# Optimization experiments

Hardware: AMD Instinct MI355X
Metric: run time of the kernel (lower is better)

The kernel has to match this reference:

```python
import jax, jax.numpy as jnp
import numpy as np

PS, R, FS, SS = 3, 2, 3, 10.0
PAD = (PS - 1) // 2  # 1


def extract_patches(x, ps, stride):
    # x: (C, Hp, Wp) already padded -> (C, ps, ps, ho, wo)
    C, Hp, Wp = x.shape
    ho = (Hp - ps) // stride + 1
    wo = (Wp - ps) // stride + 1
    rows = []
    for i in range(ps):
        cols = []
        for j in range(ps):
            cols.append(x[:, i:i + stride * ho:stride, j:j + stride * wo:stride])
        rows.append(jnp.stack(cols, axis=1))
    return jnp.stack(rows, axis=1)


def fuse_diag(S):
    # conv2d of (L,L) 'image' with eye(3) kernel, zero pad 1:
    # out[u,v] = S[u-1,v-1] + S[u,v] + S[u+1,v+1]
    Sp = jnp.pad(S, 1)
    return Sp[:-2, :-2] + Sp[1:-1, 1:-1] + Sp[2:, 2:]


def ca_single(f, b, mask):
    # f, b: (c, h, w); mask: (1, h, w)
    c, h, w = f.shape
    # full-res background patches (replicate pad, stride R) -> reconstruction bank
    b_pad = jnp.pad(b, ((0, 0), (PAD, PAD), (PAD, PAD)), mode='edge')
    bg = extract_patches(b_pad, PS, R)                 # (c,ps,ps,hr,wr)
    hr, wr = bg.shape[3], bg.shape[4]
    L = hr * wr
    bg = bg.reshape(c, PS, PS, L).transpose(3, 0, 1, 2)  # (L,c,ps,ps)
    # nearest 1/R downsample (F.interpolate nearest == strided pick)
    fl = f[:, ::R, ::R]
    bl = b[:, ::R, ::R]
    ml = mask[:, ::R, ::R]
    # shrunk background patches (replicate pad, stride 1) -> matching bank
    bl_pad = jnp.pad(bl, ((0, 0), (PAD, PAD), (PAD, PAD)), mode='edge')
    bgs = extract_patches(bl_pad, PS, 1).reshape(c, PS, PS, L).transpose(3, 0, 1, 2)
    # mask patches (zero pad), valid iff patch mean == 0
    mp = extract_patches(jnp.pad(ml, ((0, 0), (PAD, PAD), (PAD, PAD))), PS, 1)
    mi = (mp.mean(axis=(1, 2)).reshape(L) == 0.0).astype(f.dtype)  # (L,)
    # L2-normalize matching patches (clamped at 1e-4)
    bnorm = jnp.maximum(jnp.sqrt((bgs ** 2).sum(axis=(1, 2, 3))), 1e-4)
    bgs_n = bgs / bnorm[:, None, None, None]
    # score = conv2d(f, patches) with zero pad 1 -> cosine-like correlation
    fp = extract_patches(jnp.pad(fl, ((0, 0), (PAD, PAD), (PAD, PAD))), PS, 1)
    score = jnp.einsum('cijhw,lcij->lhw', fp, bgs_n)   # (L,hr,wr)
    # two-pass diagonal 'fuse' trick
    S = fuse_diag(score.reshape(L, L))
    S = S.reshape(hr, wr, hr, wr).transpose(1, 0, 3, 2).reshape(L, L)
    S = fuse_diag(S)
    score = S.reshape(wr, hr, wr, hr).transpose(1, 0, 3, 2).reshape(L, hr, wr)
    # masked softmax over the L patch axis
    score = score * mi[:, None, None]
    score = jax.nn.softmax(score * SS, axis=0) * mi[:, None, None]
    # conv_transpose2d(score, bg, stride=R, padding=PAD) / 4
    # == conv of R-dilated score with flipped kernel, pad = PS-1-PAD
    w_flip = bg[:, :, ::-1, ::-1].transpose(1, 0, 2, 3)  # (c,L,ps,ps)
    out = jax.lax.conv_general_dilated(
        score[None], w_flip, window_strides=(1, 1),
        padding=[(PS - 1 - PAD, PS - 1 - PAD)] * 2, lhs_dilation=(R, R),
        dimension_numbers=('NCHW', 'OIHW', 'NCHW'))[0] / 4.0  # (c,2hr-1,2wr-1)
    if out.shape[1] % 2 == 1:  # static shape check, matches torch branch
        out = jnp.pad(out, ((0, 0), (0, 1), (0, 1)), mode='edge')
    return out


def setup_inputs() -> dict:
    key = jax.random.key(0)
    k1, k2, k3 = jax.random.split(key, 3)
    B, c, h, w = 4, 128, 128, 128
    f = jax.random.normal(k1, (B, c, h, w), dtype=jnp.float32)
    b = jax.random.normal(k2, (B, c, h, w), dtype=jnp.float32)
    mask = jax.random.bernoulli(k3, 0.25, (B, 1, h, w)).astype(jnp.float32)
    return {'f': f, 'b': b, 'mask': mask}


def reference(f, b, mask):
    return jax.vmap(ca_single)(f, b, mask)
```

## Files before the change

### kernel.cpp

```cpp
#include <hip/hip_runtime.h>
#include <cstdint>

#define LVAL 4096
#define K1 1152
#define NT1 18
#define CCH 128
#define HH 128
#define WW 128
#define SSCALE 10.0f
#define NUPAD 2048
#define NACTPAD 512
#define PADPIX 4356
#define PIMG 557568

typedef __attribute__((ext_vector_type(8))) short short8;
typedef __attribute__((ext_vector_type(8))) _Float16 half8;
typedef __attribute__((ext_vector_type(4))) float f32x4;

static __device__ __forceinline__ int clampi(int v, int lo, int hi) {
    return v < lo ? lo : (v > hi ? hi : v);
}
static __device__ __forceinline__ unsigned short f2h(float x) {
    union { _Float16 h; unsigned short u; } c; c.h = (_Float16)x; return c.u;
}
static __device__ __forceinline__ float h2f(unsigned short u) {
    union { _Float16 h; unsigned short u; } c; c.u = u; return (float)c.h;
}

__global__ __launch_bounds__(256) void dst_kernel(const float* __restrict__ f,
        const float* __restrict__ b, unsigned short* __restrict__ fpad4,
        unsigned short* __restrict__ bpad4) {
    __shared__ float t[32][65];
    int h = blockIdx.x;
    int cg = blockIdx.y;
    int za = blockIdx.z;
    int img = za >> 1, arr = za & 1;
    const float* src = (arr ? b : f) + (size_t)img * CCH * HH * WW;
    unsigned short* dst = (arr ? bpad4 : fpad4) + (size_t)img * PIMG;
    int tid = threadIdx.x;
    int w = tid & 63, csub = tid >> 6;
    #pragma unroll
    for (int cc = 0; cc < 8; ++cc) {
        int cl = csub * 8 + cc;
        int ch = cg * 32 + cl;
        t[cl][w] = src[(size_t)ch * (HH * WW) + (2 * h) * WW + (2 * w)];
    }
    __syncthreads();
    int c = tid & 31, pr = tid >> 5;
    #pragma unroll
    for (int pp = 0; pp < 8; ++pp) {
        int w2 = pr * 8 + pp;
        dst[((size_t)(h + 1) * 66 + (w2 + 1)) * 128 + cg * 32 + c] = f2h(t[c][w2]);
    }
}

__global__ __launch_bounds__(256) void qk_border_kernel(unsigned short* __restrict__ fpad4,
        unsigned short* __restrict__ bpad4, float* __restrict__ Q) {
    int img = blockIdx.y;
    int tid = threadIdx.x;
    if (blockIdx.x < 1024) {
        int lane = tid & 63, sub = tid >> 6;
        int pix = blockIdx.x * 4 + sub;
        const unsigned short* row = bpad4 + (size_t)img * PIMG
                                    + ((size_t)((pix >> 6) + 1) * 66 + (pix & 63) + 1) * 128;
        uint32_t hv = *(const uint32_t*)(row + lane * 2);
        float a = h2f((unsigned short)(hv & 0xffff));
        float b2 = h2f((unsigned short)(hv >> 16));
        float s = a * a + b2 * b2;
        for (int off = 32; off > 0; off >>= 1) s += __shfl_xor(s, off, 64);
        if (lane == 0) Q[img * 4096 + pix] = s;
    } else {
        int id = (blockIdx.x - 1024) * 256 + tid;
        if (id >= PADPIX * 16) return;
        int pix = id >> 4, cg = (id & 15) << 3;
        int hp = pix / 66, wp = pix - hp * 66;
        if (hp >= 1 && hp <= 64 && wp >= 1 && wp <= 64) return;
        unsigned short* fp = fpad4 + (size_t)img * PIMG + (size_t)pix * 128 + cg;
        #pragma unroll
        for (int cc = 0; cc < 8; ++cc) fp[cc] = 0;
        int hs = clampi(hp - 1, 0, 63), wsx = clampi(wp - 1, 0, 63);
        const unsigned short* sb = bpad4 + (size_t)img * PIMG
                                   + ((size_t)(hs + 1) * 66 + (wsx + 1)) * 128 + cg;
        unsigned short* bp = bpad4 + (size_t)img * PIMG + (size_t)pix * 128 + cg;
        #pragma unroll
        for (int cc = 0; cc < 8; ++cc) bp[cc] = sb[cc];
    }
}

__global__ __launch_bounds__(1024) void compact_kernel(const float* __restrict__ mask,
        const float* __restrict__ Q, int* __restrict__ act, int* __restrict__ ulist,
        short* __restrict__ tapu, float* __restrict__ invn, int* __restrict__ hdr) {
    int img = blockIdx.x;
    const float* mk = mask + (size_t)img * HH * WW;
    const float* Qi = Q + img * 4096;
    int* acti = act + img * NACTPAD;
    int* uli = ulist + img * NUPAD;
    short* tpi = tapu + (size_t)img * NACTPAD * 12;
    float* invi = invn + (size_t)img * NUPAD;
    int* hd = hdr + img * 4;
    int tid = threadIdx.x;
    int lane = tid & 63, wv = tid >> 6;
    __shared__ unsigned char flag[4096];
    __shared__ short umap[4096];
    __shared__ int actl[NACTPAD];
    __shared__ float ssl[4096];
    __shared__ int wsum[16], woff[16];
    __shared__ int tot;

    int loc[4];
    int cnt = 0;
    #pragma unroll
    for (int k = 0; k < 4; ++k) {
        int a = tid * 4 + k;
        int hb = a >> 6, wb = a & 63;
        float s = 0.f;
        for (int di = -1; di <= 1; ++di)
            for (int dj = -1; dj <= 1; ++dj) {
                int hh = hb + di, w2 = wb + dj;
                if (hh >= 0 && hh < 64 && w2 >= 0 && w2 < 64)
                    s += mk[(2 * hh) * WW + 2 * w2];
            }
        loc[k] = (s == 0.f) ? 1 : 0;
        cnt += loc[k];
    }
    int pre = cnt;
    for (int off = 1; off < 64; off <<= 1) { int v = __shfl_up(pre, off, 64); if (lane >= off) pre += v; }
    if (lane == 63) wsum[wv] = pre;
    __syncthreads();
    if (tid == 0) { int a2 = 0; for (int w2 = 0; w2 < 16; ++w2) { woff[w2] = a2; a2 += wsum[w2]; } tot = a2; }
    __syncthreads();
    int base = woff[wv] + pre - cnt;
    int n_act = tot < NACTPAD ? tot : NACTPAD;
    {
        int p = base;
        #pragma unroll
        for (int k = 0; k < 4; ++k)
            if (loc[k]) { if (p < NACTPAD) { acti[p] = tid * 4 + k; actl[p] = tid * 4 + k; } p++; }
    }
    #pragma unroll
    for (int k = 0; k < 4; ++k) { flag[tid * 4 + k] = 0; umap[tid * 4 + k] = -1; }
    __syncthreads();
    for (int j = tid; j < n_act; j += 1024) {
        int a = actl[j];
        int sa = ((a & 63) << 6) + (a >> 6);
        #pragma unroll
        for (int ei = 0; ei < 3; ++ei) {
            int tbt = sa + ei - 1;
            if (tbt < 0 || tbt >= 4096) continue;
            int tb = ((tbt & 63) << 6) + (tbt >> 6);
            #pragma unroll
            for (int d = -1; d <= 1; ++d) {
                int rb = tb + d;
                if (rb >= 0 && rb < 4096) flag[rb] = 1;
            }
        }
    }
    __syncthreads();
    int cnt2 = 0;
    int loc2[4];
    #pragma unroll
    for (int k = 0; k < 4; ++k) { loc2[k] = flag[tid * 4 + k]; cnt2 += loc2[k]; }
    int pre2 = cnt2;
    for (int off = 1; off < 64; off <<= 1) { int v = __shfl_up(pre2, off, 64); if (lane >= off) pre2 += v; }
    if (lane == 63) wsum[wv] = pre2;
    __syncthreads();
    if (tid == 0) { int a2 = 0; for (int w2 = 0; w2 < 16; ++w2) { woff[w2] = a2; a2 += wsum[w2]; } tot = a2; }
    __syncthreads();
    int base2 = woff[wv] + pre2 - cnt2;
    int n_u = tot < NUPAD ? tot : NUPAD;
    {
        int p = base2;
        #pragma unroll
        for (int k = 0; k < 4; ++k)
            if (loc2[k]) { int ci = tid * 4 + k; if (p < NUPAD) { uli[p] = ci; umap[ci] = (short)p; } p++; }
    }
    __syncthreads();
    for (int j = tid; j < n_act; j += 1024) {
        int a = actl[j];
        int sa = ((a & 63) << 6) + (a >> 6);
        #pragma unroll
        for (int ei = 0; ei < 3; ++ei) {
            int tbt = sa + ei - 1;
            int ok = (tbt >= 0 && tbt < 4096);
            int tb = ok ? ((tbt & 63) << 6) + (tbt >> 6) : 0;
            #pragma unroll
            for (int d = -1; d <= 1; ++d) {
                short v = -1;
                if (ok) { int rb = tb + d; if (rb >= 0 && rb < 4096) v = umap[rb]; }
                tpi[j * 12 + ei * 3 + d + 1] = v;
            }
        }
    }
    for (int a = tid; a < 4096; a += 1024) {
        int hb = a >> 6, wb = a & 63;
        float s = 0.f;
        #pragma unroll
        for (int i = 0; i < 3; ++i)
            #pragma unroll
            for (int j2 = 0; j2 < 3; ++j2) {
                int hl = clampi(hb + i - 1, 0, 63);
                int wl = clampi(wb + j2 - 1, 0, 63);
                s += Qi[hl * 64 + wl];
            }
        ssl[a] = s;
    }
    for (int u = tid; u < NUPAD; u += 1024) invi[u] = 0.f;
    __syncthreads();
    for (int ci = tid; ci < 4096; ci += 1024) {
        if (flag[ci]) {
            int u = umap[ci];
            if (u >= 0) invi[u] = 1.f / fmaxf(sqrtf(ssl[ci]), 1e-4f);
        }
    }
    if (tid == 0) { hd[0] = n_act; hd[1] = n_u; }
}

__global__ void prep_bgtc_kernel(const float* __restrict__ b, const int* __restrict__ act,
                                 const int* __restrict__ hdr, unsigned short* __restrict__ BGTc4) {
    int gimg = blockIdx.y;
    const float* bi = b + (size_t)gimg * CCH * HH * WW;
    int idx = blockIdx.x * 256 + threadIdx.x;
    int k2 = idx >> 9, j = idx & 511;
    int n_act = hdr[gimg * 4];
    unsigned short v = 0;
    if (j < n_act) {
        int a = act[gimg * NACTPAD + j];
        int ch = k2 & 127, q = k2 >> 7;
        int i = q / 3, jj = q - i * 3;
        int y = clampi(2 * (a >> 6) + i - 1, 0, 127);
        int x = clampi(2 * (a & 63) + jj - 1, 0, 127);
        v = f2h(bi[(size_t)ch * (HH * WW) + y * WW + x]);
    }
    BGTc4[(size_t)gimg * K1 * NACTPAD + idx] = v;
}

#define BAR() __builtin_amdgcn_s_barrier()
#define WAITV6() asm volatile("s_waitcnt vmcnt(6)" ::: "memory")
#define WAITV0() asm volatile("s_waitcnt vmcnt(0)" ::: "memory")

#define STAGEX(tt, h) do {                                                              \
    int t_ = (tt);                                                                      \
    if (t_ < NT1) {                                                                     \
        const int isB_ = ((h) == 1 || (h) == 2);                                        \
        const int hi_ = ((h) >= 2) ? 1 : 0;                                             \
        int q_ = t_ >> 1;                                                               \
        int qi_ = (q_ * 11) >> 5;                                                       \
        int qj_ = q_ - qi_ * 3;                                                         \
        int toff_ = ((qi_ * 66 + qj_) << 7) + ((t_ & 1) << 6);                          \
        _Pragma("unroll")                                                               \
        for (int r_ = 0; r_ < 2; ++r_) {                                                \
            int sl_ = hi_ * 2 + r_;                                                     \
            const unsigned short* g_ = (isB_ ? bR[sl_] : aR[sl_]) + toff_;              \
            unsigned short* l_ = lds + (isB_ ? 32768 : 0) + ((t_ & 1) << 14)            \
                                 + ((hi_ * 128 + r_ * 64 + swb) << 6);                  \
            __builtin_amdgcn_global_load_lds((const uint32_t*)(const void*)g_,          \
                                             (uint32_t*)(void*)l_, 16, 0, 0);           \
        }                                                                               \
    } } while (0)

#define LDA4(cur, ah) do {                                                              \
    _Pragma("unroll")                                                                   \
    for (int f_ = 0; f_ < 4; ++f_)                                                      \
    { _Pragma("unroll")                                                                 \
      for (int s_ = 0; s_ < 2; ++s_) {                                                  \
        int row_ = wm * 128 + ((ah) * 4 + f_) * 16 + row16;                             \
        int cs_ = ((s_ << 2) + kgrp) ^ (row16 & 7);                                     \
        av[f_ * 2 + s_] = *(const half8*)(lds + ((cur) << 14) + (row_ << 6) + (cs_ << 3)); \
    } } } while (0)

#define LDB2(cur, bh) do {                                                              \
    _Pragma("unroll")                                                                   \
    for (int f_ = 0; f_ < 2; ++f_)                                                      \
    { _Pragma("unroll")                                                                 \
      for (int s_ = 0; s_ < 2; ++s_) {                                                  \
        int row_ = wn * 64 + ((bh) * 2 + f_) * 16 + row16;                              \
        int cs_ = ((s_ << 2) + kgrp) ^ (row16 & 7);                                     \
        bv[(bh) * 4 + f_ * 2 + s_] = *(const half8*)(lds + 32768 + ((cur) << 14) + (row_ << 6) + (cs_ << 3)); \
    } } } while (0)

#define MFMA16(ai, bj) do {                                                             \
    __builtin_amdgcn_s_setprio(1);                                                      \
    _Pragma("unroll")                                                                   \
    for (int f_ = 0; f_ < 4; ++f_)                                                      \
    { _Pragma("unroll")                                                                 \
      for (int g_ = 0; g_ < 2; ++g_)                                                    \
      { _Pragma("unroll")                                                               \
        for (int s_ = 0; s_ < 2; ++s_)                                                  \
            acc[(ai) * 4 + f_][(bj) * 2 + g_] = __builtin_amdgcn_mfma_f32_16x16x32_f16( \
                av[f_ * 2 + s_], bv[(bj) * 4 + g_ * 2 + s_], acc[(ai) * 4 + f_][(bj) * 2 + g_], 0, 0, 0); \
    } } __builtin_amdgcn_s_setprio(0); } while (0)

__global__ __launch_bounds__(512, 2) void gemm1_8phase(const unsigned short* __restrict__ fpad4,
        const unsigned short* __restrict__ bpad4, unsigned short* __restrict__ Scc4,
        const int* __restrict__ ulist, const int* __restrict__ hdr,
        const float* __restrict__ invn) {
    __shared__ unsigned short lds[65536];
    const int gimg = blockIdx.y;
    const unsigned short* fpadI = fpad4 + (size_t)gimg * PIMG;
    const unsigned short* bpadI = bpad4 + (size_t)gimg * PIMG;
    unsigned short* C = Scc4 + (size_t)gimg * 4096 * NUPAD;
    const int* uli = ulist + gimg * NUPAD;
    const float* invi = invn + (size_t)gimg * NUPAD;
    const int n_u = hdr[gimg * 4 + 1];
    const int tid = threadIdx.x;
    const int lane = tid & 63;
    const int wave = tid >> 6;
    const int wm = wave >> 2, wn = wave & 3;
    const int row16 = lane & 15, kgrp = lane >> 4;
    const int srow = tid >> 3, schunk = tid & 7;
    const int swb = wave << 3;
    int bid = blockIdx.x;
    int wgid = ((bid & 7) << 4) + (bid >> 3);
    const int bm = (wgid >> 3) << 8;
    const int bn = (wgid & 7) << 8;
    if (bn >= ((n_u + 255) & ~255)) return;

    const int ck8 = (schunk ^ (srow & 7)) << 3;
    const unsigned short* aR[4];
    const unsigned short* bR[4];
    #pragma unroll
    for (int i2 = 0; i2 < 4; ++i2) {
        int rowp = i2 * 64 + srow;
        int ar = bm + rowp;
        aR[i2] = fpadI + (size_t)((ar >> 6) * 66 + (ar & 63)) * 128 + ck8;
        int uu = bn + rowp;
        int brow = uli[uu < n_u ? uu : n_u - 1];
        bR[i2] = bpadI + (size_t)((brow >> 6) * 66 + (brow & 63)) * 128 + ck8;
    }

    f32x4 acc[8][4];
    #pragma unroll
    for (int i = 0; i < 8; ++i)
        #pragma unroll
        for (int j = 0; j < 4; ++j)
            acc[i][j] = (f32x4){0.f, 0.f, 0.f, 0.f};

    STAGEX(0, 1); STAGEX(0, 2); STAGEX(0, 0); STAGEX(0, 3);
    STAGEX(1, 1); STAGEX(1, 2); STAGEX(1, 0);
    WAITV6();
    BAR();

    half8 av[8], bv[8];
    for (int t = 0; t < NT1; ++t) {
        const int cur = t & 1;
        LDA4(cur, 0);
        LDB2(cur, 0);
        LDB2(cur, 1);
        STAGEX(t + 1, 3);
        BAR();
        MFMA16(0, 0);
        BAR();
        STAGEX(t + 2, 1);
        BAR();
        MFMA16(0, 1);
        BAR();
        LDA4(cur, 1);
        STAGEX(t + 2, 2);
        BAR();
        MFMA16(1, 0);
        BAR();
        STAGEX(t + 2, 0);
        BAR();
        MFMA16(1, 1);
        if (t >= NT1 - 2) { WAITV0(); } else { WAITV6(); }
        BAR();
    }

    float iv[4];
    #pragma unroll
    for (int fj = 0; fj < 4; ++fj)
        iv[fj] = invi[bn + wn * 64 + fj * 16 + row16];
    #pragma unroll
    for (int fi = 0; fi < 8; ++fi) {
        int crow = bm + wm * 128 + fi * 16 + kgrp * 4;
        #pragma unroll
        for (int fj = 0; fj < 4; ++fj) {
            int ccol = bn + wn * 64 + fj * 16 + row16;
            f32x4 v = acc[fi][fj];
            #pragma unroll
            for (int r = 0; r < 4; ++r)
                C[(size_t)(crow + r) * NUPAD + ccol] = f2h(v[r] * iv[fj]);
        }
    }
}

__global__ __launch_bounds__(512) void fuse_softmax_kernel(const unsigned short* __restrict__ Scc4,
        const int* __restrict__ hdr, const short* __restrict__ tapu,
        unsigned short* __restrict__ Pc4) {
    __shared__ unsigned short lrow[3][NUPAD];
    __shared__ float redm[8], reds[8];
    int gimg = blockIdx.y;
    const unsigned short* Scc = Scc4 + (size_t)gimg * 4096 * NUPAD;
    int bid = blockIdx.x;
    int sb = ((bid & 7) << 9) + (bid >> 3);
    int b = ((sb & 63) << 6) + (sb >> 6);
    int tid = threadIdx.x;
    int lane = tid & 63, wv = tid >> 6;
    int n_act = hdr[gimg * 4];
    int n_u = hdr[gimg * 4 + 1];
    int nu_s = (n_u + 15) & ~15;
    if (nu_s > NUPAD) nu_s = NUPAD;
    int rvalid = 0;
    int ra_[9];
    #pragma unroll
    for (int ei = 0; ei < 3; ++ei) {
        int tt = sb + ei - 1;
        int ok = (tt >= 0 && tt < 4096);
        int ta = ok ? ((tt & 63) << 6) + (tt >> 6) : 0;
        #pragma unroll
        for (int dp = 0; dp < 3; ++dp) {
            int ra = ta + dp - 1;
            int t = ei * 3 + dp;
            ra_[t] = ra;
            if (ok && ra >= 0 && ra < 4096) rvalid |= 1 << t;
        }
    }
    bool actv = tid < n_act;
    short tp[9];
    if (actv) {
        const short* tpp = tapu + ((size_t)gimg * NACTPAD + tid) * 12;
        #pragma unroll
        for (int t = 0; t < 9; ++t) tp[t] = tpp[t];
    }
    float s = 0.f;
    #pragma unroll
    for (int ei = 0; ei < 3; ++ei) {
        #pragma unroll
        for (int dp = 0; dp < 3; ++dp) {
            int t = ei * 3 + dp;
            if ((rvalid >> t) & 1) {
                const unsigned short* src = Scc + (size_t)ra_[t] * NUPAD;
                for (int u = tid * 8; u < nu_s; u += 4096)
                    *(uint4*)&lrow[dp][u] = *(const uint4*)(src + u);
            }
        }
        __syncthreads();
        if (actv) {
            #pragma unroll
            for (int dp = 0; dp < 3; ++dp) {
                int t = ei * 3 + dp;
                if ((rvalid >> t) & 1) {
                    int u = tp[t];
                    if (u >= 0) s += h2f(lrow[dp][u]);
                }
            }
        }
        __syncthreads();
    }
    float l = actv ? SSCALE * s : 0.f;
    float x = actv ? l : -3.0e38f;
    for (int off = 32; off > 0; off >>= 1) x = fmaxf(x, __shfl_xor(x, off, 64));
    if (lane == 0) redm[wv] = x;
    __syncthreads();
    float m = -3.0e38f;
    #pragma unroll
    for (int w2 = 0; w2 < 8; ++w2) m = fmaxf(m, redm[w2]);
    m = fmaxf(m, 0.f);
    float e = actv ? __expf(l - m) : 0.f;
    float sm = e;
    for (int off = 32; off > 0; off >>= 1) sm += __shfl_xor(sm, off, 64);
    if (lane == 0) reds[wv] = sm;
    __syncthreads();
    float S = 0.f;
    #pragma unroll
    for (int w2 = 0; w2 < 8; ++w2) S += reds[w2];
    float denom = S + (4096.f - (float)n_act) * __expf(-m);
    Pc4[(size_t)gimg * 4096 * NACTPAD + (size_t)b * NACTPAD + tid] = f2h(actv ? e / denom : 0.f);
}

__global__ __launch_bounds__(256) void gemm2_nt(
        const unsigned short* __restrict__ BGTc4, const unsigned short* __restrict__ Pc4,
        const int* __restrict__ hdr, unsigned short* __restrict__ OUTT4) {
    __shared__ unsigned short lds[2 * 128 * 64];
    unsigned short* Asm = lds;
    unsigned short* Bsm = lds + 128 * 64;
    const int gimg = blockIdx.z;
    const unsigned short* A = BGTc4 + (size_t)gimg * K1 * NACTPAD;
    const unsigned short* B = Pc4 + (size_t)gimg * 4096 * NACTPAD;
    unsigned short* C = OUTT4 + (size_t)gimg * K1 * LVAL;
    int n_act = hdr[gimg * 4];
    int kend = (n_act + 63) & ~63;
    if (kend < 64) kend = 64;
    const int tid = threadIdx.x;
    const int wave = tid >> 6, lane = tid & 63;
    const int wm = wave >> 1, wn = wave & 1;
    const int bm = blockIdx.y << 7, bn = blockIdx.x << 7;
    const int rsub = lane >> 3, csub = lane & 7;
    const int gcol = (csub ^ rsub) << 3;
    const int row16 = lane & 15, kgrp = lane >> 4;
    const int sw = (row16 & 7) << 3;

    f32x4 acc[4][4];
    #pragma unroll
    for (int i = 0; i < 4; ++i)
        #pragma unroll
        for (int j = 0; j < 4; ++j)
            acc[i][j] = (f32x4){0.f, 0.f, 0.f, 0.f};

    for (int k0 = 0; k0 < kend; k0 += 64) {
        __syncthreads();
        #pragma unroll
        for (int r = 0; r < 4; ++r) {
            int row = (wave << 5) + (r << 3) + rsub;
            const unsigned short* ga = A + (size_t)(bm + row) * NACTPAD + k0 + gcol;
            unsigned short* la = Asm + (((wave << 5) + (r << 3)) << 6);
            __builtin_amdgcn_global_load_lds((const uint32_t*)(const void*)ga,
                                             (uint32_t*)(void*)la, 16, 0, 0);
            const unsigned short* gb = B + (size_t)(bn + row) * NACTPAD + k0 + gcol;
            unsigned short* lb = Bsm + (((wave << 5) + (r << 3)) << 6);
            __builtin_amdgcn_global_load_lds((const uint32_t*)(const void*)gb,
                                             (uint32_t*)(void*)lb, 16, 0, 0);
        }
        __syncthreads();
        #pragma unroll
        for (int s = 0; s < 2; ++s) {
            half8 af[4], bfr[4];
            #pragma unroll
            for (int fi = 0; fi < 4; ++fi) {
                int ar = (wm << 6) + (fi << 4) + row16;
                af[fi] = *(const half8*)(Asm + (ar << 6) + (((s << 5) + (kgrp << 3)) ^ sw));
            }
            #pragma unroll
            for (int fj = 0; fj < 4; ++fj) {
                int br = (wn << 6) + (fj << 4) + row16;
                bfr[fj] = *(const half8*)(Bsm + (br << 6) + (((s << 5) + (kgrp << 3)) ^ sw));
            }
            #pragma unroll
            for (int fi = 0; fi < 4; ++fi)
                #pragma unroll
                for (int fj = 0; fj < 4; ++fj)
                    acc[fi][fj] = __builtin_amdgcn_mfma_f32_16x16x32_f16(
                        af[fi], bfr[fj], acc[fi][fj], 0, 0, 0);
        }
        __syncthreads();
    }
    #pragma unroll
    for (int fi = 0; fi < 4; ++fi) {
        int crow = bm + (wm << 6) + (fi << 4) + (kgrp << 2);
        #pragma unroll
        for (int fj = 0; fj < 4; ++fj) {
            int ccol = bn + (wn << 6) + (fj << 4) + row16;
            f32x4 v = acc[fi][fj];
            #pragma unroll
            for (int r = 0; r < 4; ++r)
                C[(size_t)(crow + r) * LVAL + ccol] = f2h(v[r]);
        }
    }
}

__global__ void scatter_kernel(const unsigned short* __restrict__ OUTT4,
                               float* __restrict__ out) {
    int gimg = blockIdx.y;
    const unsigned short* OUTT = OUTT4 + (size_t)gimg * K1 * LVAL;
    float* oi = out + (size_t)gimg * CCH * HH * WW;
    int idx = blockIdx.x * 256 + threadIdx.x;
    int x = idx & 127;
    int y = (idx >> 7) & 127;
    int ch = idx >> 14;
    int yy = y < 127 ? y : 126;
    int xx = x < 127 ? x : 126;
    int hy[2], iy[2], ny;
    if (yy & 1) { hy[0] = (yy + 1) >> 1; iy[0] = 0; hy[1] = (yy - 1) >> 1; iy[1] = 2; ny = 2; }
    else        { hy[0] = yy >> 1;       iy[0] = 1; ny = 1; }
    int wx[2], jx[2], nx;
    if (xx & 1) { wx[0] = (xx + 1) >> 1; jx[0] = 0; wx[1] = (xx - 1) >> 1; jx[1] = 2; nx = 2; }
    else        { wx[0] = xx >> 1;       jx[0] = 1; nx = 1; }
    float s = 0.f;
    for (int u = 0; u < ny; ++u)
        for (int v = 0; v < nx; ++v) {
            int k2 = (iy[u] * 3 + jx[v]) * 128 + ch;
            s += h2f(OUTT[(size_t)k2 * LVAL + (hy[u] << 6) + wx[v]]);
        }
    oi[idx] = s * 0.25f;
}

extern "C" void kernel_launch(void* const* d_in, const int* in_sizes, int n_in,
                              void* d_out, int out_size, void* d_ws, size_t ws_size,
                              hipStream_t stream) {
    const float* f = (const float*)d_in[0];
    const float* b = (const float*)d_in[1];
    const float* mask = (const float*)d_in[2];
    float* out = (float*)d_out;
    char* ws = (char*)d_ws;

    const size_t oQ    = 0;
    const size_t oACT  = 65536;
    const size_t oUL   = 73728;
    const size_t oTAP  = 106496;
    const size_t oHDR  = 155648;
    const size_t oINVN = 156672;
    const size_t oBGTC = 189440;
    const size_t oPC   = 4908032;
    const size_t oFPAD = 21685248;
    const size_t oBPAD = 26145792;
    const size_t oSCC  = 30606336;

    float* Q   = (float*)(ws + oQ);
    int*   ACT = (int*)(ws + oACT);
    int*   UL  = (int*)(ws + oUL);
    short* TAP = (short*)(ws + oTAP);
    int*   HDR = (int*)(ws + oHDR);
    float* INVN = (float*)(ws + oINVN);
    unsigned short* BGTc4 = (unsigned short*)(ws + oBGTC);
    unsigned short* Pc4   = (unsigned short*)(ws + oPC);
    unsigned short* fpad4 = (unsigned short*)(ws + oFPAD);
    unsigned short* bpad4 = (unsigned short*)(ws + oBPAD);
    unsigned short* Scc4 = (unsigned short*)(ws + oSCC);
    unsigned short* OUTT4 = (unsigned short*)(ws + oSCC);

    dst_kernel<<<dim3(64, 4, 8), 256, 0, stream>>>(f, b, fpad4, bpad4);
    qk_border_kernel<<<dim3(1297, 4), 256, 0, stream>>>(fpad4, bpad4, Q);
    compact_kernel<<<4, 1024, 0, stream>>>(mask, Q, ACT, UL, TAP, INVN, HDR);
    prep_bgtc_kernel<<<dim3(2304, 4), 256, 0, stream>>>(b, ACT, HDR, BGTc4);

    gemm1_8phase<<<dim3(128, 4), 512, 0, stream>>>(fpad4, bpad4, Scc4, UL, HDR, INVN);
    fuse_softmax_kernel<<<dim3(4096, 4), 512, 0, stream>>>(Scc4, HDR, TAP, Pc4);

    gemm2_nt<<<dim3(32, 9, 4), 256, 0, stream>>>(BGTc4, Pc4, HDR, OUTT4);
    scatter_kernel<<<dim3(8192, 4), 256, 0, stream>>>(OUTT4, out);
    (void)in_sizes; (void)n_in; (void)out_size; (void)ws_size;
}
```

Baseline: 242.8 us.

## Process four output rows per fuse-softmax block and double-buffer A fragments in gemm1

Measured after the change: 222.7 us. -8.3%, faster.

```diff
diff --git a/kernel.cpp b/kernel.cpp
--- a/kernel.cpp
+++ b/kernel.cpp
@@ -258,14 +258,14 @@
         }                                                                               \
     } } while (0)
 
-#define LDA4(cur, ah) do {                                                              \
+#define LDA4(dst, cur, ah) do {                                                         \
     _Pragma("unroll")                                                                   \
     for (int f_ = 0; f_ < 4; ++f_)                                                      \
     { _Pragma("unroll")                                                                 \
       for (int s_ = 0; s_ < 2; ++s_) {                                                  \
         int row_ = wm * 128 + ((ah) * 4 + f_) * 16 + row16;                             \
         int cs_ = ((s_ << 2) + kgrp) ^ (row16 & 7);                                     \
-        av[f_ * 2 + s_] = *(const half8*)(lds + ((cur) << 14) + (row_ << 6) + (cs_ << 3)); \
+        dst[f_ * 2 + s_] = *(const half8*)(lds + ((cur) << 14) + (row_ << 6) + (cs_ << 3)); \
     } } } while (0)
 
 #define LDB2(cur, bh) do {                                                              \
@@ -278,7 +278,7 @@
         bv[(bh) * 4 + f_ * 2 + s_] = *(const half8*)(lds + 32768 + ((cur) << 14) + (row_ << 6) + (cs_ << 3)); \
     } } } while (0)
 
-#define MFMA16(ai, bj) do {                                                             \
+#define MFMA16(va, ai, bj) do {                                                         \
     __builtin_amdgcn_s_setprio(1);                                                      \
     _Pragma("unroll")                                                                   \
     for (int f_ = 0; f_ < 4; ++f_)                                                      \
@@ -287,7 +287,7 @@
       { _Pragma("unroll")                                                               \
         for (int s_ = 0; s_ < 2; ++s_)                                                  \
             acc[(ai) * 4 + f_][(bj) * 2 + g_] = __builtin_amdgcn_mfma_f32_16x16x32_f16( \
-                av[f_ * 2 + s_], bv[(bj) * 4 + g_ * 2 + s_], acc[(ai) * 4 + f_][(bj) * 2 + g_], 0, 0, 0); \
+                va[f_ * 2 + s_], bv[(bj) * 4 + g_ * 2 + s_], acc[(ai) * 4 + f_][(bj) * 2 + g_], 0, 0, 0); \
     } } __builtin_amdgcn_s_setprio(0); } while (0)
 
 __global__ __launch_bounds__(512, 2) void gemm1_8phase(const unsigned short* __restrict__ fpad4,
@@ -340,28 +340,28 @@
     WAITV6();
     BAR();
 
-    half8 av[8], bv[8];
+    half8 av0[8], av1[8], bv[8];
     for (int t = 0; t < NT1; ++t) {
         const int cur = t & 1;
-        LDA4(cur, 0);
+        LDA4(av0, cur, 0);
         LDB2(cur, 0);
         LDB2(cur, 1);
         STAGEX(t + 1, 3);
         BAR();
-        MFMA16(0, 0);
+        MFMA16(av0, 0, 0);
+        LDA4(av1, cur, 1);
         BAR();
         STAGEX(t + 2, 1);
         BAR();
-        MFMA16(0, 1);
-        BAR();
-        LDA4(cur, 1);
+        MFMA16(av0, 0, 1);
+        BAR();
         STAGEX(t + 2, 2);
         BAR();
-        MFMA16(1, 0);
+        MFMA16(av1, 1, 0);
         BAR();
         STAGEX(t + 2, 0);
         BAR();
-        MFMA16(1, 1);
+        MFMA16(av1, 1, 1);
         if (t >= NT1 - 2) { WAITV0(); } else { WAITV6(); }
         BAR();
     }
@@ -388,33 +388,17 @@
         const int* __restrict__ hdr, const short* __restrict__ tapu,
         unsigned short* __restrict__ Pc4) {
     __shared__ unsigned short lrow[3][NUPAD];
-    __shared__ float redm[8], reds[8];
+    __shared__ float redm[8][4], reds[8][4];
     int gimg = blockIdx.y;
     const unsigned short* Scc = Scc4 + (size_t)gimg * 4096 * NUPAD;
     int bid = blockIdx.x;
-    int sb = ((bid & 7) << 9) + (bid >> 3);
-    int b = ((sb & 63) << 6) + (sb >> 6);
+    int sb0 = ((bid & 7) << 9) + ((bid >> 3) << 2);
     int tid = threadIdx.x;
     int lane = tid & 63, wv = tid >> 6;
     int n_act = hdr[gimg * 4];
     int n_u = hdr[gimg * 4 + 1];
     int nu_s = (n_u + 15) & ~15;
     if (nu_s > NUPAD) nu_s = NUPAD;
-    int rvalid = 0;
-    int ra_[9];
-    #pragma unroll
-    for (int ei = 0; ei < 3; ++ei) {
-        int tt = sb + ei - 1;
-        int ok = (tt >= 0 && tt < 4096);
-        int ta = ok ? ((tt & 63) << 6) + (tt >> 6) : 0;
-        #pragma unroll
-        for (int dp = 0; dp < 3; ++dp) {
-            int ra = ta + dp - 1;
-            int t = ei * 3 + dp;
-            ra_[t] = ra;
-            if (ok && ra >= 0 && ra < 4096) rvalid |= 1 << t;
-        }
-    }
     bool actv = tid < n_act;
     short tp[9];
     if (actv) {
@@ -422,14 +406,18 @@
         #pragma unroll
         for (int t = 0; t < 9; ++t) tp[t] = tpp[t];
     }
-    float s = 0.f;
-    #pragma unroll
-    for (int ei = 0; ei < 3; ++ei) {
+    float s[4] = {0.f, 0.f, 0.f, 0.f};
+    for (int ph = 0; ph < 6; ++ph) {
+        int tt = sb0 - 1 + ph;
+        int ok = (tt >= 0 && tt < 4096);
+        int ta = ok ? ((tt & 63) << 6) + (tt >> 6) : 0;
+        int vmask = 0;
         #pragma unroll
         for (int dp = 0; dp < 3; ++dp) {
-            int t = ei * 3 + dp;
-            if ((rvalid >> t) & 1) {
-                const unsigned short* src = Scc + (size_t)ra_[t] * NUPAD;
+            int ra = ta + dp - 1;
+            if (ok && ra >= 0 && ra < 4096) {
+                vmask |= 1 << dp;
+                const unsigned short* src = Scc + (size_t)ra * NUPAD;
                 for (int u = tid * 8; u < nu_s; u += 4096)
                     *(uint4*)&lrow[dp][u] = *(const uint4*)(src + u);
             }
@@ -437,35 +425,51 @@
         __syncthreads();
         if (actv) {
             #pragma unroll
-            for (int dp = 0; dp < 3; ++dp) {
-                int t = ei * 3 + dp;
-                if ((rvalid >> t) & 1) {
-                    int u = tp[t];
-                    if (u >= 0) s += h2f(lrow[dp][u]);
+            for (int j = 0; j < 4; ++j) {
+                int ei = ph - j;
+                if (ei >= 0 && ei < 3) {
+                    #pragma unroll
+                    for (int dp = 0; dp < 3; ++dp) {
+                        if ((vmask >> dp) & 1) {
+                            int u = tp[ei * 3 + dp];
+                            if (u >= 0) s[j] += h2f(lrow[dp][u]);
+                        }
+                    }
                 }
             }
         }
         __syncthreads();
     }
-    float l = actv ? SSCALE * s : 0.f;
-    float x = actv ? l : -3.0e38f;
-    for (int off = 32; off > 0; off >>= 1) x = fmaxf(x, __shfl_xor(x, off, 64));
-    if (lane == 0) redm[wv] = x;
-    __syncthreads();
-    float m = -3.0e38f;
-    #pragma unroll
-    for (int w2 = 0; w2 < 8; ++w2) m = fmaxf(m, redm[w2]);
-    m = fmaxf(m, 0.f);
-    float e = actv ? __expf(l - m) : 0.f;
-    float sm = e;
-    for (int off = 32; off > 0; off >>= 1) sm += __shfl_xor(sm, off, 64);
-    if (lane == 0) reds[wv] = sm;
-    __syncthreads();
-    float S = 0.f;
-    #pragma unroll
-    for (int w2 = 0; w2 < 8; ++w2) S += reds[w2];
-    float denom = S + (4096.f - (float)n_act) * __expf(-m);
-    Pc4[(size_t)gimg * 4096 * NACTPAD + (size_t)b * NACTPAD + tid] = f2h(actv ? e / denom : 0.f);
+    float m[4], e[4];
+    #pragma unroll
+    for (int j = 0; j < 4; ++j) {
+        float x = actv ? SSCALE * s[j] : -3.0e38f;
+        for (int off = 32; off > 0; off >>= 1) x = fmaxf(x, __shfl_xor(x, off, 64));
+        if (lane == 0) redm[wv][j] = x;
+    }
+    __syncthreads();
+    #pragma unroll
+    for (int j = 0; j < 4; ++j) {
+        float mm = -3.0e38f;
+        #pragma unroll
+        for (int w2 = 0; w2 < 8; ++w2) mm = fmaxf(mm, redm[w2][j]);
+        m[j] = fmaxf(mm, 0.f);
+        e[j] = actv ? __expf(SSCALE * s[j] - m[j]) : 0.f;
+        float sm = e[j];
+        for (int off = 32; off > 0; off >>= 1) sm += __shfl_xor(sm, off, 64);
+        if (lane == 0) reds[wv][j] = sm;
+    }
+    __syncthreads();
+    #pragma unroll
+    for (int j = 0; j < 4; ++j) {
+        float S = 0.f;
+        #pragma unroll
+        for (int w2 = 0; w2 < 8; ++w2) S += reds[w2][j];
+        float denom = S + (4096.f - (float)n_act) * __expf(-m[j]);
+        int sbj = sb0 + j;
+        int b = ((sbj & 63) << 6) + (sbj >> 6);
+        Pc4[(size_t)gimg * 4096 * NACTPAD + (size_t)b * NACTPAD + tid] = f2h(actv ? e[j] / denom : 0.f);
+    }
 }
 
 __global__ __launch_bounds__(256) void gemm2_nt(
@@ -614,7 +618,7 @@
     prep_bgtc_kernel<<<dim3(2304, 4), 256, 0, stream>>>(b, ACT, HDR, BGTc4);
 
     gemm1_8phase<<<dim3(128, 4), 512, 0, stream>>>(fpad4, bpad4, Scc4, UL, HDR, INVN);
-    fuse_softmax_kernel<<<dim3(4096, 4), 512, 0, stream>>>(Scc4, HDR, TAP, Pc4);
+    fuse_softmax_kernel<<<dim3(1024, 4), 512, 0, stream>>>(Scc4, HDR, TAP, Pc4);
 
     gemm2_nt<<<dim3(32, 9, 4), 256, 0, stream>>>(BGTc4, Pc4, HDR, OUTT4);
     scatter_kernel<<<dim3(8192, 4), 256, 0, stream>>>(OUTT4, out);
```
